# Kernel optimization log

Measured on AMD Instinct MI355X. Metric: run time of the kernel, lower is better.

The kernel has to match this reference:

```python
import jax, jax.numpy as jnp
import numpy as np
import math

D_MODEL = 1024
NUM_HEADS = 16
D_K = D_MODEL // NUM_HEADS
B, NQ, NK = 2, 2048, 2048


def setup_inputs() -> dict:
    key = jax.random.key(0)
    ks = jax.random.split(key, 14)
    s = 1.0 / math.sqrt(D_MODEL)
    inp = {
        "query": jax.random.normal(ks[0], (B, NQ, D_MODEL), jnp.float32),
        "key": jax.random.normal(ks[1], (B, NK, D_MODEL), jnp.float32),
        "value": jax.random.normal(ks[2], (B, NK, D_MODEL), jnp.float32),
        "mask": jax.random.randint(ks[3], (B, NK), 0, 2, jnp.int32),
        "attn_bias": jax.random.normal(ks[4], (B, NQ, NK), jnp.float32),
        "w_q": jax.random.normal(ks[5], (D_MODEL, D_MODEL), jnp.float32) * s,
        "b_q": jnp.zeros((D_MODEL,), jnp.float32),
        "w_k": jax.random.normal(ks[6], (D_MODEL, D_MODEL), jnp.float32) * s,
        "b_k": jnp.zeros((D_MODEL,), jnp.float32),
        "w_v": jax.random.normal(ks[7], (D_MODEL, D_MODEL), jnp.float32) * s,
        "b_v": jnp.zeros((D_MODEL,), jnp.float32),
        "w_o": jax.random.normal(ks[8], (D_MODEL, D_MODEL), jnp.float32) * s,
        "b_o": jnp.zeros((D_MODEL,), jnp.float32),
    }
    return inp


def reference(query, key, value, mask, attn_bias, w_q, b_q, w_k, b_k, w_v, b_v, w_o, b_o):
    # Linear projections (torch Linear: x @ W^T + b), reshape to [B, H, N, d_k]
    def proj(x, w, b, n):
        return (x @ w.T + b).reshape(x.shape[0], n, NUM_HEADS, D_K).transpose(0, 2, 1, 3)

    Q = proj(query, w_q, b_q, query.shape[1])   # [B,H,Nq,dk]
    K = proj(key, w_k, b_k, key.shape[1])       # [B,H,Nk,dk]
    V = proj(value, w_v, b_v, value.shape[1])   # [B,H,Nk,dk]

    scores = jnp.einsum("bhqd,bhkd->bhqk", Q, K) / math.sqrt(D_K)
    scores = scores + attn_bias[:, None, :, :]           # bias broadcast over heads
    pad = (mask[:, None, None, :] == 0)                   # [B,1,1,Nk]
    scores = jnp.where(pad, jnp.float32(-1e9), scores)
    attn = jax.nn.softmax(scores, axis=-1)                # dropout is identity (eval)
    out = jnp.einsum("bhqk,bhkd->bhqd", attn, V)          # [B,H,Nq,dk]
    out = out.transpose(0, 2, 1, 3).reshape(query.shape[0], query.shape[1], D_MODEL)
    return out @ w_o.T + b_o
```

## Files before the change

### kernel.cpp

```cpp
#include <hip/hip_runtime.h>


typedef short bf16x8 __attribute__((ext_vector_type(8)));
typedef short bf16x4 __attribute__((ext_vector_type(4)));
typedef float f32x4 __attribute__((ext_vector_type(4)));
typedef int i32x4 __attribute__((ext_vector_type(4)));
typedef unsigned short u16;
typedef unsigned short u16x8 __attribute__((ext_vector_type(8)));
typedef unsigned short u16x4 __attribute__((ext_vector_type(4)));

#define MFMA16(a, b, c) __builtin_amdgcn_mfma_f32_16x16x32_bf16((a), (b), (c), 0, 0, 0)
#define GLD16(gp, lp)                                                     \
  __builtin_amdgcn_global_load_lds(                                       \
      (const __attribute__((address_space(1))) void*)(gp),                \
      (__attribute__((address_space(3))) void*)(lp), 16, 0, 0)

#define WAITVM_BAR(N) asm volatile("s_waitcnt vmcnt(" #N ")\ns_barrier" ::: "memory")
#define BAR() asm volatile("s_barrier" ::: "memory")

#if __has_builtin(__builtin_amdgcn_exp2f)
#define EXP2(x) __builtin_amdgcn_exp2f(x)
#else
#define EXP2(x) exp2f(x)
#endif

__device__ __forceinline__ f32x4 MFMA_PV(bf16x4 a, bf16x4 b, f32x4 c) {
#if __has_builtin(__builtin_amdgcn_mfma_f32_16x16x16bf16_1k)
  return __builtin_amdgcn_mfma_f32_16x16x16bf16_1k(a, b, c, 0, 0, 0);
#else
  asm("v_mfma_f32_16x16x16_bf16 %0, %1, %2, %0" : "+v"(c) : "v"(a), "v"(b));
  return c;
#endif
}

__device__ __forceinline__ u16 f2bf(float f) {
  union { float f; unsigned u; } v; v.f = f;
  return (u16)((v.u + 0x7fffu + ((v.u >> 16) & 1u)) >> 16);
}
__device__ __forceinline__ unsigned pk2(float x, float y) {
  union { float f; unsigned u; } a, b;
  a.f = x; b.f = y;
  return ((a.u + 0x8000u) >> 16) | ((b.u + 0x8000u) & 0xffff0000u);
}

struct ConvDesc { const float* src; u16* dst; int n; };
struct ConvArgs { ConvDesc d[7]; };

__device__ __forceinline__ void biasprep_body(const float* __restrict__ bias,
                                              const int* __restrict__ mask,
                                              u16* __restrict__ out, int i) {
  const int o0 = i * 16;
  const int rowg = o0 >> 11;
  const int b = rowg >> 11;
  const int off = o0 & 2047;
  const int a = off >> 6, g = (off >> 4) & 3;
  const float* src = bias + (size_t)rowg * 2048 + a * 64 + g * 4;
  const int* msk = mask + b * 2048 + a * 64 + g * 4;
  u16x8 w0 = {}, w1 = {};
#pragma unroll
  for (int c = 0; c < 4; c++) {
    f32x4 v = *(const f32x4*)(src + c * 16);
    i32x4 m = *(const i32x4*)(msk + c * 16);
#pragma unroll
    for (int j = 0; j < 4; j++) {
      u16 val = (m[j] != 0) ? f2bf(v[j] * 1.44269504f) : (u16)0xFF80;
      if (c < 2) w0[c * 4 + j] = val;
      else       w1[(c - 2) * 4 + j] = val;
    }
  }
  *(u16x8*)(out + o0) = w0;
  *(u16x8*)(out + o0 + 8) = w1;
}

__global__ __launch_bounds__(256)
void k_prep(ConvArgs a, const float* __restrict__ bias,
            const int* __restrict__ mask, u16* __restrict__ bout) {
  if (blockIdx.y == 7) {
    biasprep_body(bias, mask, bout, blockIdx.x * 256 + threadIdx.x);
    return;
  }
  ConvDesc cd = a.d[blockIdx.y];
  int i = (blockIdx.x * 256 + threadIdx.x) * 8;
  if (i >= cd.n) return;
  const float4* s = (const float4*)(cd.src + i);
  float4 f0 = s[0], f1 = s[1];
  u16x8 o;
  o[0] = f2bf(f0.x); o[1] = f2bf(f0.y); o[2] = f2bf(f0.z); o[3] = f2bf(f0.w);
  o[4] = f2bf(f1.x); o[5] = f2bf(f1.y); o[6] = f2bf(f1.z); o[7] = f2bf(f1.w);
  *(u16x8*)(cd.dst + i) = o;
}

__global__ __launch_bounds__(256)
void k_biasprep(const float* __restrict__ bias, const int* __restrict__ mask,
                u16* __restrict__ out) {
  biasprep_body(bias, mask, out, blockIdx.x * 256 + threadIdx.x);
}

template <int MF>
__device__ __forceinline__ void gemm_impl(const u16* __restrict__ A,
                                          const u16* __restrict__ Bw,
                                          const float* __restrict__ bias,
                                          void* __restrict__ outp, int mode,
                                          float oscale) {
  __shared__ u16 As[2][MF * 1024];
  __shared__ u16 Bs[2][4096];
  const int tid = threadIdx.x;
  const int lane = tid & 63;
  const int wv = tid >> 6;
  const int wr = wv >> 1, wc = wv & 1;
  const int m0 = blockIdx.y * (MF * 32), n0 = blockIdx.x * 128;

  f32x4 acc[MF][4] = {};

  const int s0 = tid, s1 = 256 + tid;
  const int r0 = s0 >> 2, c0 = (s0 & 3) ^ (r0 & 3);
  const int r1 = s1 >> 2, c1 = (s1 & 3) ^ (r1 & 3);
  const u16* gA0 = A + (size_t)(m0 + r0) * 1024 + c0 * 8;
  const u16* gA1 = A + (size_t)(m0 + r1) * 1024 + c1 * 8;
  const u16* gB0 = Bw + (size_t)(n0 + r0) * 1024 + c0 * 8;
  const u16* gB1 = Bw + (size_t)(n0 + r1) * 1024 + c1 * 8;
  u16* lA0 = &As[0][(tid & ~63) * 8];
  u16* lB0 = &Bs[0][(tid & ~63) * 8];

  GLD16(gA0, lA0);
  if constexpr (MF == 4) GLD16(gA1, lA0 + 2048);
  GLD16(gB0, lB0);
  GLD16(gB1, lB0 + 2048);
  WAITVM_BAR(0);

#define GSTEP(BUF, K0)                                                     \
  {                                                                        \
    const int nk = ((K0) + 32) & 1023;                                     \
    GLD16(gA0 + nk, lA0 + ((BUF) ^ 1) * (MF * 1024));                      \
    if constexpr (MF == 4)                                                 \
      GLD16(gA1 + nk, lA0 + 2048 + ((BUF) ^ 1) * (MF * 1024));             \
    GLD16(gB0 + nk, lB0 + ((BUF) ^ 1) * 4096);                             \
    GLD16(gB1 + nk, lB0 + 2048 + ((BUF) ^ 1) * 4096);                      \
    if constexpr (MF == 4) { WAITVM_BAR(4); } else { WAITVM_BAR(3); }      \
    bf16x8 af[MF], bfr[4];                                                 \
    _Pragma("unroll")                                                      \
    for (int mi = 0; mi < MF; mi++) {                                      \
      int row = wr * (MF * 16) + mi * 16 + (lane & 15);                    \
      int byt = row * 64 + (((lane >> 4) * 16) ^ ((row & 3) << 4));        \
      af[mi] = *(const bf16x8*)((const char*)&As[BUF][0] + byt);           \
    }                                                                      \
    _Pragma("unroll")                                                      \
    for (int ni = 0; ni < 4; ni++) {                                       \
      int row = wc * 64 + ni * 16 + (lane & 15);                           \
      int byt = row * 64 + (((lane >> 4) * 16) ^ ((row & 3) << 4));        \
      bfr[ni] = *(const bf16x8*)((const char*)&Bs[BUF][0] + byt);          \
    }                                                                      \
    __builtin_amdgcn_s_setprio(1);                                         \
    _Pragma("unroll")                                                      \
    for (int mi = 0; mi < MF; mi++)                                        \
      _Pragma("unroll")                                                    \
      for (int ni = 0; ni < 4; ni++)                                       \
        acc[mi][ni] = MFMA16(af[mi], bfr[ni], acc[mi][ni]);                \
    __builtin_amdgcn_s_setprio(0);                                         \
    BAR();                                                                 \
  }

  for (int k0 = 0; k0 < 1024; k0 += 64) {
    GSTEP(0, k0)
    GSTEP(1, k0 + 32)
  }
#undef GSTEP

#pragma unroll
  for (int ni = 0; ni < 4; ni++) {
    int n = n0 + wc * 64 + ni * 16 + (lane & 15);
    float bv = bias[n];
#pragma unroll
    for (int mi = 0; mi < MF; mi++) {
      int mb = m0 + wr * (MF * 16) + mi * 16 + (lane >> 4) * 4;
      if (mode == 2) {
        float* O = (float*)outp;
#pragma unroll
        for (int r = 0; r < 4; r++)
          O[(size_t)(mb + r) * 1024 + n] = (acc[mi][ni][r] + bv) * oscale;
      } else if (mode == 0) {
        u16* O = (u16*)outp;
        int b = mb >> 11, q = mb & 2047;
        int h = n >> 6, dk = n & 63;
        size_t base = ((size_t)(b * 16 + h) * 2048 + q) * 64 + dk;
#pragma unroll
        for (int r = 0; r < 4; r++)
          O[base + (size_t)r * 64] = f2bf((acc[mi][ni][r] + bv) * oscale);
      } else {
        u16* O = (u16*)outp;
        int b = mb >> 11, kv = mb & 2047;
        int h = n >> 6, dk = n & 63;
        u16x4 pk;
#pragma unroll
        for (int r = 0; r < 4; r++) pk[r] = f2bf((acc[mi][ni][r] + bv) * oscale);
        *(u16x4*)((u16*)O + ((size_t)((b * 16 + h) * 64 + dk)) * 2048 + kv) = pk;
      }
    }
  }
}

struct GemmDesc { const u16* A; const u16* W; const float* bias; void* out;
                  int mode; float oscale; };
struct Gemm3 { GemmDesc d[3]; };

__global__ __launch_bounds__(256, 2) void k_gemm_qkv(Gemm3 g3) {
  GemmDesc gd = g3.d[blockIdx.z];
  gemm_impl<4>(gd.A, gd.W, gd.bias, gd.out, gd.mode, gd.oscale);
}
__global__ __launch_bounds__(256, 2)
void k_gemm_o(const u16* __restrict__ A, const u16* __restrict__ W,
              const float* __restrict__ bias, float* __restrict__ out) {
  gemm_impl<2>(A, W, bias, out, 2, 1.0f);
}

__global__ __launch_bounds__(256, 2)
void k_attn(const u16* __restrict__ Qb, const u16* __restrict__ Kb,
            const u16* __restrict__ Vt, const u16* __restrict__ BiasE,
            u16* __restrict__ Ob) {
  __shared__ u16 Ks[2][64 * 64];
  __shared__ u16 Vs[2][64 * 64];

  const int tid = threadIdx.x, lane = tid & 63, w = tid >> 6;
  const int g = lane >> 4, q = lane & 15;
  const int h = blockIdx.x, b = blockIdx.y, qt = blockIdx.z;
  const int q0 = qt * 128;
  const size_t bh = (size_t)(b * 16 + h);

  bf16x8 bq0[2], bq1[2];
#pragma unroll
  for (int s = 0; s < 2; s++) {
    const u16* Qrow = Qb + (bh * 2048 + q0 + w * 32 + s * 16 + q) * 64;
    bq0[s] = *(const bf16x8*)(Qrow + g * 8);
    bq1[s] = *(const bf16x8*)(Qrow + 32 + g * 8);
  }

  f32x4 acc[2][4] = {};
  float mrun[2] = {-1e30f, -1e30f}, lrun[2] = {0.f, 0.f};

  const int sA = tid, sB = tid + 256;
  const int r0 = sA >> 3, c0 = (sA & 7) ^ (r0 & 7);
  const int r1 = sB >> 3, c1 = (sB & 7) ^ (r1 & 7);
  const u16* Kg = Kb + bh * 2048 * 64;
  const u16* Vg = Vt + bh * 64 * 2048;
  const int ld0 = (tid & ~63) * 8, ld1 = ld0 + 2048;

  const u16* brow[2];
#pragma unroll
  for (int s = 0; s < 2; s++)
    brow[s] = BiasE + ((size_t)b * 2048 + q0 + w * 32 + s * 16 + q) * 2048 + g * 16;

  GLD16(Kg + (size_t)r0 * 64 + c0 * 8, &Ks[0][ld0]);
  GLD16(Kg + (size_t)r1 * 64 + c1 * 8, &Ks[0][ld1]);
  GLD16(Vg + (size_t)r0 * 2048 + c0 * 8, &Vs[0][ld0]);
  GLD16(Vg + (size_t)r1 * 2048 + c1 * 8, &Vs[0][ld1]);
  WAITVM_BAR(0);
  u16x8 bbA[2][2], bbB[2][2];
#pragma unroll
  for (int s = 0; s < 2; s++) {
    bbA[s][0] = *(const u16x8*)(brow[s]);
    bbA[s][1] = *(const u16x8*)(brow[s] + 8);
  }

#define ATTN_STEP(BUF, BBU, BBF, T)                                           \
  {                                                                           \
    const int nkv = (((T) + 1) & 31) * 64;                                    \
    GLD16(Kg + (size_t)(nkv + r0) * 64 + c0 * 8, &Ks[(BUF) ^ 1][ld0]);        \
    GLD16(Kg + (size_t)(nkv + r1) * 64 + c1 * 8, &Ks[(BUF) ^ 1][ld1]);        \
    GLD16(Vg + (size_t)r0 * 2048 + nkv + c0 * 8, &Vs[(BUF) ^ 1][ld0]);        \
    GLD16(Vg + (size_t)r1 * 2048 + nkv + c1 * 8, &Vs[(BUF) ^ 1][ld1]);        \
    _Pragma("unroll")                                                         \
    for (int s = 0; s < 2; s++) {                                             \
      BBF[s][0] = *(const u16x8*)(brow[s] + nkv);                             \
      BBF[s][1] = *(const u16x8*)(brow[s] + nkv + 8);                         \
    }                                                                         \
    WAITVM_BAR(8);                                                            \
    f32x4 sc[2][4];                                                           \
    __builtin_amdgcn_s_setprio(1);                                            \
    _Pragma("unroll")                                                         \
    for (int c = 0; c < 4; c++) {                                             \
      const int kvr = c * 16 + q;                                             \
      bf16x8 ak0 = *(const bf16x8*)((const char*)&Ks[BUF][0] + kvr * 128 +    \
                                    ((g * 16) ^ ((kvr & 7) << 4)));           \
      bf16x8 ak1 = *(const bf16x8*)((const char*)&Ks[BUF][0] + kvr * 128 +    \
                                    ((64 + g * 16) ^ ((kvr & 7) << 4)));      \
      _Pragma("unroll")                                                       \
      for (int s = 0; s < 2; s++) {                                           \
        f32x4 z = {};                                                         \
        z = MFMA16(ak0, bq0[s], z);                                           \
        z = MFMA16(ak1, bq1[s], z);                                           \
        sc[s][c] = z;                                                         \
      }                                                                       \
    }                                                                         \
    __builtin_amdgcn_s_setprio(0);                                            \
    float p[2][4][4];                                                         \
    float tmax[2] = {-3e38f, -3e38f};                                         \
    _Pragma("unroll")                                                         \
    for (int s = 0; s < 2; s++) {                                             \
      _Pragma("unroll")                                                       \
      for (int c = 0; c < 4; c++)                                             \
        _Pragma("unroll")                                                     \
        for (int r = 0; r < 4; r++) {                                         \
          unsigned braw =                                                     \
              (unsigned)(c < 2 ? (BBU)[s][0][c * 4 + r]                       \
                               : (BBU)[s][1][(c - 2) * 4 + r]);               \
          float sv = sc[s][c][r] + __uint_as_float(braw << 16);               \
          p[s][c][r] = sv;                                                    \
          tmax[s] = fmaxf(tmax[s], sv);                                       \
        }                                                                     \
      tmax[s] = fmaxf(tmax[s], __shfl_xor(tmax[s], 16, 64));                  \
      tmax[s] = fmaxf(tmax[s], __shfl_xor(tmax[s], 32, 64));                  \
    }                                                                         \
    if (__any((tmax[0] > mrun[0]) | (tmax[1] > mrun[1]))) {                   \
      _Pragma("unroll")                                                       \
      for (int s = 0; s < 2; s++) {                                           \
        float mnew = fmaxf(mrun[s], tmax[s]);                                 \
        float alpha = EXP2(mrun[s] - mnew);                                   \
        mrun[s] = mnew;                                                       \
        lrun[s] *= alpha;                                                     \
        _Pragma("unroll")                                                     \
        for (int j = 0; j < 4; j++) {                                         \
          float aj = __shfl(alpha, g * 4 + j, 64);                            \
          _Pragma("unroll")                                                   \
          for (int d = 0; d < 4; d++) acc[s][d][j] *= aj;                     \
        }                                                                     \
      }                                                                       \
    }                                                                         \
    _Pragma("unroll")                                                         \
    for (int s = 0; s < 2; s++) {                                             \
      float rsum = 0.f;                                                       \
      _Pragma("unroll")                                                       \
      for (int c = 0; c < 4; c++)                                             \
        _Pragma("unroll")                                                     \
        for (int r = 0; r < 4; r++) {                                         \
          p[s][c][r] = EXP2(p[s][c][r] - mrun[s]);                            \
          rsum += p[s][c][r];                                                 \
        }                                                                     \
      rsum += __shfl_xor(rsum, 16, 64);                                       \
      rsum += __shfl_xor(rsum, 32, 64);                                       \
      lrun[s] += rsum;                                                        \
    }                                                                         \
    __builtin_amdgcn_s_setprio(1);                                            \
    _Pragma("unroll")                                                         \
    for (int c = 0; c < 4; c++) {                                             \
      union { unsigned u[2]; bf16x4 v; } pa[2];                               \
      _Pragma("unroll")                                                       \
      for (int s = 0; s < 2; s++) {                                           \
        pa[s].u[0] = pk2(p[s][c][0], p[s][c][1]);                             \
        pa[s].u[1] = pk2(p[s][c][2], p[s][c][3]);                             \
      }                                                                       \
      _Pragma("unroll")                                                       \
      for (int d = 0; d < 4; d++) {                                           \
        const int dr = d * 16 + q;                                            \
        bf16x4 vb = *(const bf16x4*)((const char*)&Vs[BUF][0] + dr * 128 +    \
                                     ((c * 32 + g * 8) ^ ((dr & 7) << 4)));   \
        _Pragma("unroll")                                                     \
        for (int s = 0; s < 2; s++) acc[s][d] = MFMA_PV(pa[s].v, vb, acc[s][d]); \
      }                                                                       \
    }                                                                         \
    __builtin_amdgcn_s_setprio(0);                                            \
    BAR();                                                                    \
  }

  for (int t = 0; t < 32; t += 2) {
    ATTN_STEP(0, bbA, bbB, t)
    ATTN_STEP(1, bbB, bbA, t + 1)
  }
#undef ATTN_STEP

#pragma unroll
  for (int s = 0; s < 2; s++) {
    float linv = 1.0f / lrun[s];
#pragma unroll
    for (int j = 0; j < 4; j++) {
      float li = __shfl(linv, g * 4 + j, 64);
      int qq = q0 + w * 32 + s * 16 + g * 4 + j;
#pragma unroll
      for (int d = 0; d < 4; d++)
        Ob[((size_t)b * 2048 + qq) * 1024 + h * 64 + d * 16 + q] =
            f2bf(acc[s][d][j] * li);
    }
  }
}

extern "C" void kernel_launch(void* const* d_in, const int* in_sizes, int n_in,
                              void* d_out, int out_size, void* d_ws,
                              size_t ws_size, hipStream_t stream) {
  (void)in_sizes; (void)n_in; (void)out_size;
  const float* q_in = (const float*)d_in[0];
  const float* k_in = (const float*)d_in[1];
  const float* v_in = (const float*)d_in[2];
  const int* mask = (const int*)d_in[3];
  const float* attn_bias = (const float*)d_in[4];
  const float* w_q = (const float*)d_in[5];
  const float* b_q = (const float*)d_in[6];
  const float* w_k = (const float*)d_in[7];
  const float* b_k = (const float*)d_in[8];
  const float* w_v = (const float*)d_in[9];
  const float* b_v = (const float*)d_in[10];
  const float* w_o = (const float*)d_in[11];
  const float* b_o = (const float*)d_in[12];

  const size_t MB = 1u << 20;
  char* ws = (char*)d_ws;
  u16* XQ = (u16*)(ws + 0 * MB);
  u16* XK = (u16*)(ws + 8 * MB);
  u16* XV = (u16*)(ws + 16 * MB);
  u16* WQ = (u16*)(ws + 24 * MB);
  u16* WK = (u16*)(ws + 26 * MB);
  u16* WV = (u16*)(ws + 28 * MB);
  u16* WO = (u16*)(ws + 30 * MB);
  u16* Qb = (u16*)(ws + 32 * MB);
  u16* Kb = (u16*)(ws + 40 * MB);
  u16* Vt = (u16*)(ws + 48 * MB);
  u16* Ob = (u16*)(ws + 56 * MB);
  const bool merged = ws_size >= (size_t)80 * MB;
  u16* BiasE = (u16*)(ws + (merged ? 64 : 0) * MB);

  ConvArgs ca;
  ca.d[0] = {q_in, XQ, 4096 * 1024};
  ca.d[1] = {k_in, XK, 4096 * 1024};
  ca.d[2] = {v_in, XV, 4096 * 1024};
  ca.d[3] = {w_q, WQ, 1024 * 1024};
  ca.d[4] = {w_k, WK, 1024 * 1024};
  ca.d[5] = {w_v, WV, 1024 * 1024};
  ca.d[6] = {w_o, WO, 1024 * 1024};
  k_prep<<<dim3(2048, merged ? 8 : 7), 256, 0, stream>>>(ca, attn_bias, mask,
                                                         BiasE);

  const float QSCALE = 0.125f * 1.44269504f;
  Gemm3 g3;
  g3.d[0] = {XQ, WQ, b_q, (void*)Qb, 0, QSCALE};
  g3.d[1] = {XK, WK, b_k, (void*)Kb, 0, 1.0f};
  g3.d[2] = {XV, WV, b_v, (void*)Vt, 1, 1.0f};
  k_gemm_qkv<<<dim3(8, 32, 3), 256, 0, stream>>>(g3);

  if (!merged) k_biasprep<<<2048, 256, 0, stream>>>(attn_bias, mask, BiasE);

  k_attn<<<dim3(16, 2, 16), 256, 0, stream>>>(Qb, Kb, Vt, BiasE, Ob);

  k_gemm_o<<<dim3(8, 64), 256, 0, stream>>>(Ob, WO, b_o, (float*)d_out);
}
```

Measured before the change: 169.3 us.

## Use 8 waves per attention block with 16 query rows per wave

The attention kernel now launches 512 threads per block, and each of the 8 waves owns 16 query rows instead of 32. Each thread issues one K and one V load per tile instead of two, so the shared-memory fill is spread across more threads. Register use per thread falls (one accumulator set, one softmax state), which allows higher occupancy via launch bounds (512,4) and better latency hiding. The cost is that each K/V fragment read from LDS now feeds half as many MFMAs, which raises LDS traffic per FLOP, and more waves contend at each barrier.

Measured after the change: 160.9 us. -4.9%, faster.

```diff
diff --git a/kernel.cpp b/kernel.cpp
--- a/kernel.cpp
+++ b/kernel.cpp
@@ -213,7 +213,7 @@
   gemm_impl<2>(A, W, bias, out, 2, 1.0f);
 }
 
-__global__ __launch_bounds__(256, 2)
+__global__ __launch_bounds__(512, 4)
 void k_attn(const u16* __restrict__ Qb, const u16* __restrict__ Kb,
             const u16* __restrict__ Vt, const u16* __restrict__ BiasE,
             u16* __restrict__ Ob) {
@@ -226,135 +226,100 @@
   const int q0 = qt * 128;
   const size_t bh = (size_t)(b * 16 + h);
 
-  bf16x8 bq0[2], bq1[2];
-#pragma unroll
-  for (int s = 0; s < 2; s++) {
-    const u16* Qrow = Qb + (bh * 2048 + q0 + w * 32 + s * 16 + q) * 64;
-    bq0[s] = *(const bf16x8*)(Qrow + g * 8);
-    bq1[s] = *(const bf16x8*)(Qrow + 32 + g * 8);
-  }
-
-  f32x4 acc[2][4] = {};
-  float mrun[2] = {-1e30f, -1e30f}, lrun[2] = {0.f, 0.f};
-
-  const int sA = tid, sB = tid + 256;
-  const int r0 = sA >> 3, c0 = (sA & 7) ^ (r0 & 7);
-  const int r1 = sB >> 3, c1 = (sB & 7) ^ (r1 & 7);
+  const u16* Qrow = Qb + (bh * 2048 + q0 + w * 16 + q) * 64;
+  bf16x8 bq0 = *(const bf16x8*)(Qrow + g * 8);
+  bf16x8 bq1 = *(const bf16x8*)(Qrow + 32 + g * 8);
+
+  f32x4 acc[4] = {};
+  float mrun = -1e30f, lrun = 0.f;
+
+  const int r0 = tid >> 3, c0 = (tid & 7) ^ (r0 & 7);
   const u16* Kg = Kb + bh * 2048 * 64;
   const u16* Vg = Vt + bh * 64 * 2048;
-  const int ld0 = (tid & ~63) * 8, ld1 = ld0 + 2048;
-
-  const u16* brow[2];
-#pragma unroll
-  for (int s = 0; s < 2; s++)
-    brow[s] = BiasE + ((size_t)b * 2048 + q0 + w * 32 + s * 16 + q) * 2048 + g * 16;
+  const int ld0 = (tid & ~63) * 8;
+
+  const u16* brow = BiasE + ((size_t)b * 2048 + q0 + w * 16 + q) * 2048 + g * 16;
 
   GLD16(Kg + (size_t)r0 * 64 + c0 * 8, &Ks[0][ld0]);
-  GLD16(Kg + (size_t)r1 * 64 + c1 * 8, &Ks[0][ld1]);
   GLD16(Vg + (size_t)r0 * 2048 + c0 * 8, &Vs[0][ld0]);
-  GLD16(Vg + (size_t)r1 * 2048 + c1 * 8, &Vs[0][ld1]);
   WAITVM_BAR(0);
-  u16x8 bbA[2][2], bbB[2][2];
-#pragma unroll
-  for (int s = 0; s < 2; s++) {
-    bbA[s][0] = *(const u16x8*)(brow[s]);
-    bbA[s][1] = *(const u16x8*)(brow[s] + 8);
-  }
-
-#define ATTN_STEP(BUF, BBU, BBF, T)                                           \
+  u16x8 bbA0 = *(const u16x8*)(brow);
+  u16x8 bbA1 = *(const u16x8*)(brow + 8);
+  u16x8 bbB0 = {}, bbB1 = {};
+
+#define ATTN_STEP(BUF, B0, B1, NB0, NB1, T)                                   \
   {                                                                           \
     const int nkv = (((T) + 1) & 31) * 64;                                    \
     GLD16(Kg + (size_t)(nkv + r0) * 64 + c0 * 8, &Ks[(BUF) ^ 1][ld0]);        \
-    GLD16(Kg + (size_t)(nkv + r1) * 64 + c1 * 8, &Ks[(BUF) ^ 1][ld1]);        \
     GLD16(Vg + (size_t)r0 * 2048 + nkv + c0 * 8, &Vs[(BUF) ^ 1][ld0]);        \
-    GLD16(Vg + (size_t)r1 * 2048 + nkv + c1 * 8, &Vs[(BUF) ^ 1][ld1]);        \
-    _Pragma("unroll")                                                         \
-    for (int s = 0; s < 2; s++) {                                             \
-      BBF[s][0] = *(const u16x8*)(brow[s] + nkv);                             \
-      BBF[s][1] = *(const u16x8*)(brow[s] + nkv + 8);                         \
-    }                                                                         \
-    WAITVM_BAR(8);                                                            \
-    f32x4 sc[2][4];                                                           \
+    NB0 = *(const u16x8*)(brow + nkv);                                        \
+    NB1 = *(const u16x8*)(brow + nkv + 8);                                    \
+    WAITVM_BAR(4);                                                            \
+    f32x4 sc[4];                                                              \
     __builtin_amdgcn_s_setprio(1);                                            \
     _Pragma("unroll")                                                         \
     for (int c = 0; c < 4; c++) {                                             \
       const int kvr = c * 16 + q;                                             \
+      f32x4 z = {};                                                           \
       bf16x8 ak0 = *(const bf16x8*)((const char*)&Ks[BUF][0] + kvr * 128 +    \
                                     ((g * 16) ^ ((kvr & 7) << 4)));           \
       bf16x8 ak1 = *(const bf16x8*)((const char*)&Ks[BUF][0] + kvr * 128 +    \
                                     ((64 + g * 16) ^ ((kvr & 7) << 4)));      \
+      z = MFMA16(ak0, bq0, z);                                                \
+      z = MFMA16(ak1, bq1, z);                                                \
+      sc[c] = z;                                                              \
+    }                                                                         \
+    __builtin_amdgcn_s_setprio(0);                                            \
+    float p[4][4];                                                            \
+    float tmax = -3e38f;                                                      \
+    _Pragma("unroll")                                                         \
+    for (int c = 0; c < 4; c++) {                                             \
       _Pragma("unroll")                                                       \
-      for (int s = 0; s < 2; s++) {                                           \
-        f32x4 z = {};                                                         \
-        z = MFMA16(ak0, bq0[s], z);                                           \
-        z = MFMA16(ak1, bq1[s], z);                                           \
-        sc[s][c] = z;                                                         \
+      for (int r = 0; r < 4; r++) {                                           \
+        unsigned braw =                                                       \
+            (unsigned)(c < 2 ? (B0)[c * 4 + r] : (B1)[(c - 2) * 4 + r]);      \
+        float s = sc[c][r] + __uint_as_float(braw << 16);                     \
+        p[c][r] = s;                                                          \
+        tmax = fmaxf(tmax, s);                                                \
       }                                                                       \
     }                                                                         \
-    __builtin_amdgcn_s_setprio(0);                                            \
-    float p[2][4][4];                                                         \
-    float tmax[2] = {-3e38f, -3e38f};                                         \
-    _Pragma("unroll")                                                         \
-    for (int s = 0; s < 2; s++) {                                             \
+    tmax = fmaxf(tmax, __shfl_xor(tmax, 16, 64));                             \
+    tmax = fmaxf(tmax, __shfl_xor(tmax, 32, 64));                             \
+    if (__any(tmax > mrun)) {                                                 \
+      float mnew = fmaxf(mrun, tmax);                                         \
+      float alpha = EXP2(mrun - mnew);                                        \
+      mrun = mnew;                                                            \
+      lrun *= alpha;                                                          \
       _Pragma("unroll")                                                       \
-      for (int c = 0; c < 4; c++)                                             \
+      for (int j = 0; j < 4; j++) {                                           \
+        float aj = __shfl(alpha, g * 4 + j, 64);                              \
         _Pragma("unroll")                                                     \
-        for (int r = 0; r < 4; r++) {                                         \
-          unsigned braw =                                                     \
-              (unsigned)(c < 2 ? (BBU)[s][0][c * 4 + r]                       \
-                               : (BBU)[s][1][(c - 2) * 4 + r]);               \
-          float sv = sc[s][c][r] + __uint_as_float(braw << 16);               \
-          p[s][c][r] = sv;                                                    \
-          tmax[s] = fmaxf(tmax[s], sv);                                       \
-        }                                                                     \
-      tmax[s] = fmaxf(tmax[s], __shfl_xor(tmax[s], 16, 64));                  \
-      tmax[s] = fmaxf(tmax[s], __shfl_xor(tmax[s], 32, 64));                  \
-    }                                                                         \
-    if (__any((tmax[0] > mrun[0]) | (tmax[1] > mrun[1]))) {                   \
-      _Pragma("unroll")                                                       \
-      for (int s = 0; s < 2; s++) {                                           \
-        float mnew = fmaxf(mrun[s], tmax[s]);                                 \
-        float alpha = EXP2(mrun[s] - mnew);                                   \
-        mrun[s] = mnew;                                                       \
-        lrun[s] *= alpha;                                                     \
-        _Pragma("unroll")                                                     \
-        for (int j = 0; j < 4; j++) {                                         \
-          float aj = __shfl(alpha, g * 4 + j, 64);                            \
-          _Pragma("unroll")                                                   \
-          for (int d = 0; d < 4; d++) acc[s][d][j] *= aj;                     \
-        }                                                                     \
+        for (int d = 0; d < 4; d++) acc[d][j] *= aj;                          \
       }                                                                       \
     }                                                                         \
+    float rsum = 0.f;                                                         \
     _Pragma("unroll")                                                         \
-    for (int s = 0; s < 2; s++) {                                             \
-      float rsum = 0.f;                                                       \
+    for (int c = 0; c < 4; c++)                                               \
       _Pragma("unroll")                                                       \
-      for (int c = 0; c < 4; c++)                                             \
-        _Pragma("unroll")                                                     \
-        for (int r = 0; r < 4; r++) {                                         \
-          p[s][c][r] = EXP2(p[s][c][r] - mrun[s]);                            \
-          rsum += p[s][c][r];                                                 \
-        }                                                                     \
-      rsum += __shfl_xor(rsum, 16, 64);                                       \
-      rsum += __shfl_xor(rsum, 32, 64);                                       \
-      lrun[s] += rsum;                                                        \
-    }                                                                         \
+      for (int r = 0; r < 4; r++) {                                           \
+        p[c][r] = EXP2(p[c][r] - mrun);                                       \
+        rsum += p[c][r];                                                      \
+      }                                                                       \
+    rsum += __shfl_xor(rsum, 16, 64);                                         \
+    rsum += __shfl_xor(rsum, 32, 64);                                         \
+    lrun += rsum;                                                             \
     __builtin_amdgcn_s_setprio(1);                                            \
     _Pragma("unroll")                                                         \
     for (int c = 0; c < 4; c++) {                                             \
-      union { unsigned u[2]; bf16x4 v; } pa[2];                               \
-      _Pragma("unroll")                                                       \
-      for (int s = 0; s < 2; s++) {                                           \
-        pa[s].u[0] = pk2(p[s][c][0], p[s][c][1]);                             \
-        pa[s].u[1] = pk2(p[s][c][2], p[s][c][3]);                             \
-      }                                                                       \
+      union { unsigned u[2]; bf16x4 v; } pa;                                  \
+      pa.u[0] = pk2(p[c][0], p[c][1]);                                        \
+      pa.u[1] = pk2(p[c][2], p[c][3]);                                        \
       _Pragma("unroll")                                                       \
       for (int d = 0; d < 4; d++) {                                           \
         const int dr = d * 16 + q;                                            \
         bf16x4 vb = *(const bf16x4*)((const char*)&Vs[BUF][0] + dr * 128 +    \
                                      ((c * 32 + g * 8) ^ ((dr & 7) << 4)));   \
-        _Pragma("unroll")                                                     \
-        for (int s = 0; s < 2; s++) acc[s][d] = MFMA_PV(pa[s].v, vb, acc[s][d]); \
+        acc[d] = MFMA_PV(pa.v, vb, acc[d]);                                   \
       }                                                                       \
     }                                                                         \
     __builtin_amdgcn_s_setprio(0);                                            \
@@ -362,23 +327,20 @@
   }
 
   for (int t = 0; t < 32; t += 2) {
-    ATTN_STEP(0, bbA, bbB, t)
-    ATTN_STEP(1, bbB, bbA, t + 1)
+    ATTN_STEP(0, bbA0, bbA1, bbB0, bbB1, t)
+    ATTN_STEP(1, bbB0, bbB1, bbA0, bbA1, t + 1)
   }
 #undef ATTN_STEP
 
-#pragma unroll
-  for (int s = 0; s < 2; s++) {
-    float linv = 1.0f / lrun[s];
-#pragma unroll
-    for (int j = 0; j < 4; j++) {
-      float li = __shfl(linv, g * 4 + j, 64);
-      int qq = q0 + w * 32 + s * 16 + g * 4 + j;
-#pragma unroll
-      for (int d = 0; d < 4; d++)
-        Ob[((size_t)b * 2048 + qq) * 1024 + h * 64 + d * 16 + q] =
-            f2bf(acc[s][d][j] * li);
-    }
+  float linv = 1.0f / lrun;
+#pragma unroll
+  for (int j = 0; j < 4; j++) {
+    float li = __shfl(linv, g * 4 + j, 64);
+    int qq = q0 + w * 16 + g * 4 + j;
+#pragma unroll
+    for (int d = 0; d < 4; d++)
+      Ob[((size_t)b * 2048 + qq) * 1024 + h * 64 + d * 16 + q] =
+          f2bf(acc[d][j] * li);
   }
 }
 
@@ -436,7 +398,7 @@
 
   if (!merged) k_biasprep<<<2048, 256, 0, stream>>>(attn_bias, mask, BiasE);
 
-  k_attn<<<dim3(16, 2, 16), 256, 0, stream>>>(Qb, Kb, Vt, BiasE, Ob);
+  k_attn<<<dim3(16, 2, 16), 512, 0, stream>>>(Qb, Kb, Vt, BiasE, Ob);
 
   k_gemm_o<<<dim3(8, 64), 256, 0, stream>>>(Ob, WO, b_o, (float*)d_out);
 }
```
